# Kernel tuning notes

Measured on AMD Instinct MI355X. Metric: run time of the kernel, lower is better.

Reference implementation:

```python
import jax, jax.numpy as jnp
import numpy as np

N, L, BAG_NUM, NUM_CLASSES = 131072, 512, 512, 128
BIG_NEG = 65535.0  # matches torch code's (1-indicator)*65535 mask


def setup_inputs() -> dict:
    key = jax.random.key(0)
    k1, k2, k3, k4, k5 = jax.random.split(key, 5)
    H = jax.random.normal(k1, (N, L), dtype=jnp.float32)
    attention = jax.random.normal(k2, (1, N), dtype=jnp.float32)
    batch = jnp.sort(jax.random.randint(k3, (N,), 0, BAG_NUM)).astype(jnp.int64)
    fc1_w = jax.random.normal(k4, (NUM_CLASSES, L), dtype=jnp.float32) * 0.02
    fc1_b = jax.random.normal(k5, (NUM_CLASSES,), dtype=jnp.float32) * 0.02
    return {"H": H, "attention": attention, "batch": batch, "fc1_w": fc1_w, "fc1_b": fc1_b}


def reference(H, attention, batch, fc1_w, fc1_b):
    # pool_model='attention', paradigm='embedding'
    # indicator: (N, BAG_NUM) one-hot bag membership
    indicator = jax.nn.one_hot(batch, BAG_NUM, dtype=H.dtype)
    # A: broadcast per-instance attention score into its bag column
    A = attention.T * indicator                      # (N, BAG_NUM)
    # per-bag softmax over instances (dim 0), non-members pushed to -65535
    A = jax.nn.softmax(A - (1.0 - indicator) * BIG_NEG, axis=0)
    bag_feat = A.T @ H                               # (BAG_NUM, L)
    return bag_feat @ fc1_w.T + fc1_b                # (BAG_NUM, NUM_CLASSES)
```

## Files before the change

kernel.cpp:

```cpp
#include <hip/hip_runtime.h>
#include <math.h>

#define N_INST 131072
#define L_DIM 512
#define BAG_NUM 512
#define NUM_CLASSES 128
#define CHUNK 1024

__global__ __launch_bounds__(256) void bag_fused_kernel(
        const float* __restrict__ H, const float* __restrict__ att,
        const int* __restrict__ batch, const float* __restrict__ fc1_w,
        const float* __restrict__ fc1_b, float* __restrict__ out) {
    int b = blockIdx.x;
    int tid = threadIdx.x;

    int s, e;
    {
        int lo = 0, hi = N_INST;
        while (lo < hi) {
            int mid = (lo + hi) >> 1;
            if (batch[mid] < b) lo = mid + 1; else hi = mid;
        }
        s = lo;
        hi = N_INST;
        while (lo < hi) {
            int mid = (lo + hi) >> 1;
            if (batch[mid] < b + 1) lo = mid + 1; else hi = mid;
        }
        e = lo;
    }

    __shared__ float red[8];
    __shared__ float wlds[CHUNK];
    __shared__ float row[L_DIM];

    float m = -3.4e38f;
    for (int i = s + tid; i < e; i += 256) m = fmaxf(m, att[i]);
    for (int off = 32; off >= 1; off >>= 1) m = fmaxf(m, __shfl_down(m, off));
    if ((tid & 63) == 0) red[tid >> 6] = m;
    __syncthreads();
    m = fmaxf(fmaxf(red[0], red[1]), fmaxf(red[2], red[3]));

    float sum = 0.f;
    for (int i = s + tid; i < e; i += 256) sum += expf(att[i] - m);
    for (int off = 32; off >= 1; off >>= 1) sum += __shfl_down(sum, off);
    if ((tid & 63) == 0) red[4 + (tid >> 6)] = sum;
    __syncthreads();
    float inv = 1.0f / (red[4] + red[5] + red[6] + red[7]);

    float ax = 0.f, ay = 0.f;
    const float2* __restrict__ H2 = (const float2*)H;
    for (int c0 = s; c0 < e; c0 += CHUNK) {
        int ce = min(c0 + CHUNK, e);
        __syncthreads();
        for (int i = c0 + tid; i < ce; i += 256)
            wlds[i - c0] = expf(att[i] - m) * inv;
        __syncthreads();
        int i = c0;
        for (; i + 8 <= ce; i += 8) {
            float w[8];
            float2 h[8];
#pragma unroll
            for (int j = 0; j < 8; ++j) w[j] = wlds[i - c0 + j];
#pragma unroll
            for (int j = 0; j < 8; ++j)
                h[j] = H2[(size_t)(i + j) * 256 + tid];
#pragma unroll
            for (int j = 0; j < 8; ++j) {
                ax = fmaf(w[j], h[j].x, ax);
                ay = fmaf(w[j], h[j].y, ay);
            }
        }
        for (; i < ce; ++i) {
            float w = wlds[i - c0];
            float2 h = H2[(size_t)i * 256 + tid];
            ax = fmaf(w, h.x, ax);
            ay = fmaf(w, h.y, ay);
        }
    }

    ((float2*)row)[tid] = make_float2(ax, ay);
    __syncthreads();
    if (tid < NUM_CLASSES) {
        const float4* __restrict__ w4 = (const float4*)(fc1_w + (size_t)tid * L_DIM);
        float acc = fc1_b[tid];
#pragma unroll 8
        for (int k4 = 0; k4 < L_DIM / 4; ++k4) {
            float4 wv = w4[k4];
            float4 rv = *(const float4*)(row + 4 * k4);
            acc = fmaf(wv.x, rv.x, acc);
            acc = fmaf(wv.y, rv.y, acc);
            acc = fmaf(wv.z, rv.z, acc);
            acc = fmaf(wv.w, rv.w, acc);
        }
        out[(size_t)b * NUM_CLASSES + tid] = acc;
    }
}

extern "C" void kernel_launch(void* const* d_in, const int* in_sizes, int n_in,
                              void* d_out, int out_size, void* d_ws, size_t ws_size,
                              hipStream_t stream) {
    const float* H     = (const float*)d_in[0];
    const float* att   = (const float*)d_in[1];
    const int*   batch = (const int*)d_in[2];
    const float* fc1_w = (const float*)d_in[3];
    const float* fc1_b = (const float*)d_in[4];
    float* out = (float*)d_out;

    bag_fused_kernel<<<BAG_NUM, 256, 0, stream>>>(H, att, batch, fc1_w, fc1_b, out);
}
```

Before: 388.5 us.

## Precompute bag boundaries and use float4 loads over two row-halves

Adds a small pre-kernel that computes the start index of every bag from the sorted batch array, replacing two per-block binary searches. The main kernel now loads H with float4 per thread, so each half of the block processes alternating rows, and the halves are combined through shared memory. The fc1 matvec is split across all 256 threads with a shared-memory reduction. This adds a second launch and extra synchronisation in exchange for wider memory loads and fewer latency-bound searches.

New measurement: 383.2 us. Within noise of the previous version (-1.4%).

```diff
diff --git a/kernel.cpp b/kernel.cpp
--- a/kernel.cpp
+++ b/kernel.cpp
@@ -7,32 +7,33 @@
 #define NUM_CLASSES 128
 #define CHUNK 1024
 
+__global__ void boundaries_kernel(const int* __restrict__ batch,
+                                  int* __restrict__ start) {
+    int i = blockIdx.x * blockDim.x + threadIdx.x;
+    if (i >= N_INST) return;
+    int b = batch[i];
+    int prev = (i == 0) ? -1 : batch[i - 1];
+    for (int bb = prev + 1; bb <= b; ++bb) start[bb] = i;
+    if (i == N_INST - 1) {
+        for (int bb = b + 1; bb <= BAG_NUM; ++bb) start[bb] = N_INST;
+    }
+}
+
 __global__ __launch_bounds__(256) void bag_fused_kernel(
         const float* __restrict__ H, const float* __restrict__ att,
-        const int* __restrict__ batch, const float* __restrict__ fc1_w,
+        const int* __restrict__ start, const float* __restrict__ fc1_w,
         const float* __restrict__ fc1_b, float* __restrict__ out) {
     int b = blockIdx.x;
     int tid = threadIdx.x;
+    int c = tid & 127;
+    int p = tid >> 7;
 
-    int s, e;
-    {
-        int lo = 0, hi = N_INST;
-        while (lo < hi) {
-            int mid = (lo + hi) >> 1;
-            if (batch[mid] < b) lo = mid + 1; else hi = mid;
-        }
-        s = lo;
-        hi = N_INST;
-        while (lo < hi) {
-            int mid = (lo + hi) >> 1;
-            if (batch[mid] < b + 1) lo = mid + 1; else hi = mid;
-        }
-        e = lo;
-    }
+    int s = start[b], e = start[b + 1];
 
     __shared__ float red[8];
     __shared__ float wlds[CHUNK];
-    __shared__ float row[L_DIM];
+    __shared__ float4 cmb[128];
+    __shared__ float fcred[256];
 
     float m = -3.4e38f;
     for (int i = s + tid; i < e; i += 256) m = fmaxf(m, att[i]);
@@ -48,8 +49,8 @@
     __syncthreads();
     float inv = 1.0f / (red[4] + red[5] + red[6] + red[7]);
 
-    float ax = 0.f, ay = 0.f;
-    const float2* __restrict__ H2 = (const float2*)H;
+    float4 acc = make_float4(0.f, 0.f, 0.f, 0.f);
+    const float4* __restrict__ H4 = (const float4*)H;
     for (int c0 = s; c0 < e; c0 += CHUNK) {
         int ce = min(c0 + CHUNK, e);
         __syncthreads();
@@ -57,44 +58,70 @@
             wlds[i - c0] = expf(att[i] - m) * inv;
         __syncthreads();
         int i = c0;
-        for (; i + 8 <= ce; i += 8) {
+        for (; i + 16 <= ce; i += 16) {
             float w[8];
-            float2 h[8];
+            float4 h[8];
 #pragma unroll
-            for (int j = 0; j < 8; ++j) w[j] = wlds[i - c0 + j];
+            for (int j = 0; j < 8; ++j) w[j] = wlds[i - c0 + p + 2 * j];
 #pragma unroll
             for (int j = 0; j < 8; ++j)
-                h[j] = H2[(size_t)(i + j) * 256 + tid];
+                h[j] = H4[(size_t)(i + p + 2 * j) * 128 + c];
 #pragma unroll
             for (int j = 0; j < 8; ++j) {
-                ax = fmaf(w[j], h[j].x, ax);
-                ay = fmaf(w[j], h[j].y, ay);
+                acc.x = fmaf(w[j], h[j].x, acc.x);
+                acc.y = fmaf(w[j], h[j].y, acc.y);
+                acc.z = fmaf(w[j], h[j].z, acc.z);
+                acc.w = fmaf(w[j], h[j].w, acc.w);
             }
         }
-        for (; i < ce; ++i) {
+        for (; i + 2 <= ce; i += 2) {
+            float w = wlds[i - c0 + p];
+            float4 h = H4[(size_t)(i + p) * 128 + c];
+            acc.x = fmaf(w, h.x, acc.x);
+            acc.y = fmaf(w, h.y, acc.y);
+            acc.z = fmaf(w, h.z, acc.z);
+            acc.w = fmaf(w, h.w, acc.w);
+        }
+        if (i < ce && p == 0) {
             float w = wlds[i - c0];
-            float2 h = H2[(size_t)i * 256 + tid];
-            ax = fmaf(w, h.x, ax);
-            ay = fmaf(w, h.y, ay);
+            float4 h = H4[(size_t)i * 128 + c];
+            acc.x = fmaf(w, h.x, acc.x);
+            acc.y = fmaf(w, h.y, acc.y);
+            acc.z = fmaf(w, h.z, acc.z);
+            acc.w = fmaf(w, h.w, acc.w);
         }
     }
 
-    ((float2*)row)[tid] = make_float2(ax, ay);
+    if (p == 1) cmb[c] = acc;
     __syncthreads();
-    if (tid < NUM_CLASSES) {
-        const float4* __restrict__ w4 = (const float4*)(fc1_w + (size_t)tid * L_DIM);
-        float acc = fc1_b[tid];
+    if (p == 0) {
+        float4 o = cmb[c];
+        o.x += acc.x; o.y += acc.y; o.z += acc.z; o.w += acc.w;
+        cmb[c] = o;
+    }
+    __syncthreads();
+
+    {
+        const float* rowf = (const float*)cmb;
+        const float4* __restrict__ w4 =
+            (const float4*)(fc1_w + (size_t)c * L_DIM + p * 256);
+        const float4* __restrict__ r4 = (const float4*)(rowf + p * 256);
+        float a = 0.f;
 #pragma unroll 8
-        for (int k4 = 0; k4 < L_DIM / 4; ++k4) {
+        for (int k4 = 0; k4 < 64; ++k4) {
             float4 wv = w4[k4];
-            float4 rv = *(const float4*)(row + 4 * k4);
-            acc = fmaf(wv.x, rv.x, acc);
-            acc = fmaf(wv.y, rv.y, acc);
-            acc = fmaf(wv.z, rv.z, acc);
-            acc = fmaf(wv.w, rv.w, acc);
+            float4 rv = r4[k4];
+            a = fmaf(wv.x, rv.x, a);
+            a = fmaf(wv.y, rv.y, a);
+            a = fmaf(wv.z, rv.z, a);
+            a = fmaf(wv.w, rv.w, a);
         }
-        out[(size_t)b * NUM_CLASSES + tid] = acc;
+        fcred[tid] = a;
     }
+    __syncthreads();
+    if (tid < NUM_CLASSES)
+        out[(size_t)b * NUM_CLASSES + tid] =
+            fcred[tid] + fcred[tid + 128] + fc1_b[tid];
 }
 
 extern "C" void kernel_launch(void* const* d_in, const int* in_sizes, int n_in,
@@ -107,5 +134,8 @@
     const float* fc1_b = (const float*)d_in[4];
     float* out = (float*)d_out;
 
-    bag_fused_kernel<<<BAG_NUM, 256, 0, stream>>>(H, att, batch, fc1_w, fc1_b, out);
+    int* start = (int*)d_ws;
+
+    boundaries_kernel<<<N_INST / 256, 256, 0, stream>>>(batch, start);
+    bag_fused_kernel<<<BAG_NUM, 256, 0, stream>>>(H, att, start, fc1_w, fc1_b, out);
 }
```
